# Performance work log

Measured on AMD Instinct MI355X. Metric: run time of the kernel, lower is better.

Reference implementation:

```python
import jax, jax.numpy as jnp
import numpy as np
from jax import lax

B, T, H, L = 8192, 1, 1024, 4  # batch, decode steps, hidden_size, n_layers


def _lstm_layer(c, h, xs, Wx, Wh, b):
    """Uni-directional LSTM over time axis. xs: [B, T, F]; c,h: [B, H].
    Returns final carry (c, h) and per-step hidden states [B, T, H]."""
    def step(carry, x_t):
        c, h = carry
        z = x_t @ Wx + h @ Wh + b              # [B, 4H]
        i, f, g, o = jnp.split(z, 4, axis=-1)
        i = jax.nn.sigmoid(i)
        f = jax.nn.sigmoid(f)
        g = jnp.tanh(g)
        o = jax.nn.sigmoid(o)
        c = f * c + i * g
        h = o * jnp.tanh(c)
        return (c, h), h
    (c, h), hs = lax.scan(step, (c, h), jnp.swapaxes(xs, 0, 1))  # scan over T
    return c, h, jnp.swapaxes(hs, 0, 1)        # [B, T, H]


def setup_inputs() -> dict:
    key = jax.random.key(0)
    ks = jax.random.split(key, 12)
    s = 0.02
    return {
        "x_todec": jax.random.normal(ks[0], (B, T), jnp.float32),
        "c0": jax.random.normal(ks[1], (B, H), jnp.float32),
        "h0": jax.random.normal(ks[2], (B, H), jnp.float32),
        # layer 0: input feature dim = 1 (x_todec expanded on axis 2)
        "Wx0": jax.random.normal(ks[3], (1, 4 * H), jnp.float32) * s,
        "Wh0": jax.random.normal(ks[4], (H, 4 * H), jnp.float32) * s,
        "b0": jnp.zeros((4 * H,), jnp.float32),
        # layers 1..L-1: input feature dim = H
        "Wx": jax.random.normal(ks[5], (L - 1, H, 4 * H), jnp.float32) * s,
        "Wh": jax.random.normal(ks[6], (L - 1, H, 4 * H), jnp.float32) * s,
        "b": jnp.zeros((L - 1, 4 * H), jnp.float32),
        # final prediction head Dense(features=1)
        "Wd": jax.random.normal(ks[7], (H, 1), jnp.float32) * s,
        "bd": jnp.zeros((1,), jnp.float32),
        "training": 0,
    }


def reference(x_todec, c0, h0, Wx0, Wh0, b0, Wx, Wh, b, Wd, bd, training):
    # training=0 -> nn.Dropout deterministic -> identity; omitted.
    x = x_todec[..., None]                      # [B, T, 1]
    c, h, xs = _lstm_layer(c0, h0, x, Wx0, Wh0, b0)
    for l in range(L - 1):                      # carry chains through layers
        c, h, xs = _lstm_layer(c, h, xs, Wx[l], Wh[l], b[l])
    x_pred = jnp.squeeze(xs @ Wd + bd, axis=-1)  # [B, T]
    return (c, h, x_pred)
```

## Files before the change

### kernel.cpp

```cpp
#include <hip/hip_runtime.h>
#include <hip/hip_bf16.h>


#define MB_  8192
#define HB_  1024
#define KB_  1024

typedef __attribute__((ext_vector_type(8))) short bf16x8;
typedef __attribute__((ext_vector_type(4))) float f32x4;

#define BAR()  asm volatile("s_barrier" ::: "memory")
#define VMW(n) asm volatile("s_waitcnt vmcnt(" #n ")" ::: "memory")

__device__ __forceinline__ void load_lds16(const void* g, void* l) {
  __builtin_amdgcn_global_load_lds(
      (const __attribute__((address_space(1))) unsigned int*)g,
      (__attribute__((address_space(3))) unsigned int*)l, 16, 0, 0);
}

__device__ __forceinline__ float sigmoidf_(float x) { return 1.0f / (1.0f + __expf(-x)); }
__device__ __forceinline__ float tanhf_fast(float x) { return 2.0f / (1.0f + __expf(-2.0f * x)) - 1.0f; }

__device__ __forceinline__ short f2bf(float f) {
  __hip_bfloat16 h = __float2bfloat16(f);
  return *(short*)&h;
}

__global__ __launch_bounds__(256) void cvt_f32_bf16(
    const float* __restrict__ in, __hip_bfloat16* __restrict__ out)
{
  const int i = blockIdx.x * 256 + threadIdx.x;
  const float4 f0 = ((const float4*)in)[i * 2];
  const float4 f1 = ((const float4*)in)[i * 2 + 1];
  bf16x8 v;
  v[0] = f2bf(f0.x); v[1] = f2bf(f0.y); v[2] = f2bf(f0.z); v[3] = f2bf(f0.w);
  v[4] = f2bf(f1.x); v[5] = f2bf(f1.y); v[6] = f2bf(f1.z); v[7] = f2bf(f1.w);
  ((bf16x8*)out)[i] = v;
}

__global__ __launch_bounds__(256) void prep_weights(
    const float* __restrict__ Wh0,
    const float* __restrict__ Wx,
    const float* __restrict__ Wh,
    __hip_bfloat16* __restrict__ WT)
{
  __shared__ float t[32][33];
  const int L  = blockIdx.z;
  const int n0 = blockIdx.x * 32;
  const int k0 = blockIdx.y * 32;
  const int tx = threadIdx.x & 31;
  const int ty = threadIdx.x >> 5;
  if (L == 0) {
    for (int kk = ty; kk < 32; kk += 8)
      t[kk][tx] = Wh0[(size_t)(k0 + kk) * 4096 + n0 + tx];
  } else {
    const float* wx = Wx + (size_t)(L - 1) * 1024 * 4096;
    const float* wh = Wh + (size_t)(L - 1) * 1024 * 4096;
    for (int kk = ty; kk < 32; kk += 8) {
      size_t idx = (size_t)(k0 + kk) * 4096 + n0 + tx;
      t[kk][tx] = wx[idx] + wh[idx];
    }
  }
  __syncthreads();
  __hip_bfloat16* dst = WT + (size_t)L * 4096 * 1024;
  for (int nn = ty; nn < 32; nn += 8)
    dst[(size_t)(n0 + nn) * 1024 + k0 + tx] = __float2bfloat16(t[tx][nn]);
}

template<bool FIRST, bool LAST>
__global__ __launch_bounds__(512, 2) void lstm_layer_kernel(
    const __hip_bfloat16* __restrict__ A,
    const __hip_bfloat16* __restrict__ WT,
    const float*          __restrict__ bias,
    const float*                       cin,
    float*                             cout,
    const float*          __restrict__ xvec,
    const float*          __restrict__ Wx0,
    void*                 __restrict__ hout)
{
  __shared__ __align__(16) char lds[131072];

  const int tid  = threadIdx.x;
  const int lane = tid & 63;
  const int wv   = tid >> 6;
  const int wr   = wv & 1;
  const int wc   = wv >> 1;
  const int l15  = lane & 15;
  const int lq   = lane >> 4;
  const int sw   = (l15 & 7) << 4;

  const int bid = blockIdx.x;
  const int sz  = (bid & 7) * 64 + (bid >> 3);
  const int m0  = (sz >> 4) * 256;
  const int n0h = (sz & 15) * 64;

  unsigned aoff[2][2], boff[2][2];
#pragma unroll
  for (int h = 0; h < 2; ++h)
#pragma unroll
    for (int j = 0; j < 2; ++j) {
      const int c    = j * 512 + tid;
      const int row  = c >> 3;
      const int colb = ((c & 7) ^ (row & 7)) << 4;
      aoff[h][j] = (unsigned)((m0 + h * 128 + row) * 2048 + colb);
      const int grow = (h * 2 + (row >> 6)) * 1024 + n0h + (row & 63);
      boff[h][j] = (unsigned)(grow * 2048 + colb);
    }
  const int ldsu = wv * 1024;
  const char* Ab = (const char*)A;
  const char* Wb = (const char*)WT;

  f32x4 acc[8][4] = {};

  auto stageA = [&](int h, int kt, int b) {
#pragma unroll
    for (int j = 0; j < 2; ++j)
      load_lds16(Ab + aoff[h][j] + kt * 128,
                 lds + b * 65536 + h * 16384 + j * 8192 + ldsu);
  };
  auto stageB = [&](int h, int kt, int b) {
#pragma unroll
    for (int j = 0; j < 2; ++j)
      load_lds16(Wb + boff[h][j] + kt * 128,
                 lds + b * 65536 + 32768 + h * 16384 + j * 8192 + ldsu);
  };
  auto quad = [&](int b, int sh, int gh) {
    const char* bA = lds + b * 65536 + wr * 16384;
    const char* bB = lds + b * 65536 + 32768 + gh * 16384;
    bf16x8 af[4][2], bfr[2][2];
#pragma unroll
    for (int i = 0; i < 4; ++i) {
      const int rl = (sh * 4 + i) * 16 + l15;
#pragma unroll
      for (int ks = 0; ks < 2; ++ks)
        af[i][ks] = *(const bf16x8*)(bA + rl * 128 + ((ks * 64 + lq * 16) ^ sw));
    }
#pragma unroll
    for (int g = 0; g < 2; ++g) {
      const int rb = g * 64 + wc * 16 + l15;
#pragma unroll
      for (int ks = 0; ks < 2; ++ks)
        bfr[g][ks] = *(const bf16x8*)(bB + rb * 128 + ((ks * 64 + lq * 16) ^ sw));
    }
    __builtin_amdgcn_s_setprio(1);
#pragma unroll
    for (int i = 0; i < 4; ++i)
#pragma unroll
      for (int g = 0; g < 2; ++g)
#pragma unroll
        for (int ks = 0; ks < 2; ++ks)
          acc[sh * 4 + i][gh * 2 + g] = __builtin_amdgcn_mfma_f32_16x16x32_bf16(
              af[i][ks], bfr[g][ks], acc[sh * 4 + i][gh * 2 + g], 0, 0, 0);
    __builtin_amdgcn_s_setprio(0);
  };

  stageA(0, 0, 0); stageA(1, 0, 0); stageB(0, 0, 0); stageB(1, 0, 0);

  for (int t = 0; t < 15; ++t) {
    const int cur = t & 1, nxt = cur ^ 1;
    VMW(2); BAR();
    stageA(0, t + 1, nxt); stageA(1, t + 1, nxt);
    quad(cur, 0, 0);
    BAR();
    stageB(0, t + 1, nxt);
    quad(cur, 1, 0);
    VMW(6); BAR();
    stageB(1, t + 1, nxt);
    quad(cur, 0, 1);
    BAR();
    quad(cur, 1, 1);
  }
  VMW(2); BAR();
  quad(1, 0, 0);
  quad(1, 1, 0);
  VMW(0); BAR();
  quad(1, 0, 1);
  quad(1, 1, 1);

  BAR();
  float* sC = (float*)lds;
  float* sH = (float*)(lds + 65536);

#pragma unroll
  for (int j = 0; j < 8; ++j) {
    const int idx = j * 512 + tid;
    const int row = idx >> 4;
    const int c4  = (idx & 15) << 2;
    load_lds16(cin + (size_t)(m0 + row) * HB_ + n0h + c4,
               (char*)sC + j * 8192 + ldsu);
  }

  const int jj  = n0h + wc * 16 + l15;
  const float bi  = bias[0 * HB_ + jj];
  const float bf_ = bias[1 * HB_ + jj];
  const float bg  = bias[2 * HB_ + jj];
  const float bo  = bias[3 * HB_ + jj];
  float wxi = 0.f, wxf = 0.f, wxg = 0.f, wxo = 0.f;
  if (FIRST) {
    wxi = Wx0[0 * HB_ + jj];
    wxf = Wx0[1 * HB_ + jj];
    wxg = Wx0[2 * HB_ + jj];
    wxo = Wx0[3 * HB_ + jj];
  }
  VMW(0); BAR();

  const int hl = wc * 16 + l15;
#pragma unroll
  for (int s = 0; s < 8; ++s) {
#pragma unroll
    for (int r = 0; r < 4; ++r) {
      const int mloc = wr * 128 + s * 16 + (lq << 2) + r;
      float zi = acc[s][0][r] + bi;
      float zf = acc[s][1][r] + bf_;
      float zg = acc[s][2][r] + bg;
      float zo = acc[s][3][r] + bo;
      if (FIRST) {
        const float xv = xvec[m0 + mloc];
        zi += xv * wxi; zf += xv * wxf; zg += xv * wxg; zo += xv * wxo;
      }
      const float ig = sigmoidf_(zi);
      const float fg = sigmoidf_(zf);
      const float gg = tanhf_fast(zg);
      const float og = sigmoidf_(zo);
      const float cn = fg * sC[mloc * 64 + hl] + ig * gg;
      const float hn = og * tanhf_fast(cn);
      sC[mloc * 64 + hl] = cn;
      sH[mloc * 64 + hl] = hn;
    }
  }
  BAR();

#pragma unroll
  for (int p = 0; p < 8; ++p) {
    const int idx = p * 512 + tid;
    const int row = idx >> 4, seg = idx & 15;
    *(float4*)(cout + (size_t)(m0 + row) * HB_ + n0h + seg * 4) =
        *(const float4*)&sC[row * 64 + seg * 4];
  }
  if (LAST) {
#pragma unroll
    for (int p = 0; p < 8; ++p) {
      const int idx = p * 512 + tid;
      const int row = idx >> 4, seg = idx & 15;
      *(float4*)((float*)hout + (size_t)(m0 + row) * HB_ + n0h + seg * 4) =
          *(const float4*)&sH[row * 64 + seg * 4];
    }
  } else {
#pragma unroll
    for (int p = 0; p < 4; ++p) {
      const int idx = p * 512 + tid;
      const int row = idx >> 3, seg = idx & 7;
      const float4 f0 = *(const float4*)&sH[row * 64 + seg * 8];
      const float4 f1 = *(const float4*)&sH[row * 64 + seg * 8 + 4];
      bf16x8 v;
      v[0] = f2bf(f0.x); v[1] = f2bf(f0.y); v[2] = f2bf(f0.z); v[3] = f2bf(f0.w);
      v[4] = f2bf(f1.x); v[5] = f2bf(f1.y); v[6] = f2bf(f1.z); v[7] = f2bf(f1.w);
      *(bf16x8*)((__hip_bfloat16*)hout + (size_t)(m0 + row) * HB_ + n0h + seg * 8) = v;
    }
  }
}

__global__ __launch_bounds__(256) void head_kernel(
    const float* __restrict__ h,
    const float* __restrict__ Wd,
    const float* __restrict__ bd,
    float* __restrict__ xpred)
{
  const int row  = blockIdx.x * 4 + (threadIdx.x >> 6);
  const int lane = threadIdx.x & 63;
  const float* hr = h + (size_t)row * HB_;
  float s = 0.f;
#pragma unroll
  for (int t = 0; t < 16; ++t) {
    const int k = t * 64 + lane;
    s += hr[k] * Wd[k];
  }
#pragma unroll
  for (int off = 32; off; off >>= 1) s += __shfl_down(s, off, 64);
  if (lane == 0) xpred[row] = s + bd[0];
}

extern "C" void kernel_launch(void* const* d_in, const int* in_sizes, int n_in,
                              void* d_out, int out_size, void* d_ws, size_t ws_size,
                              hipStream_t stream) {
  (void)in_sizes; (void)n_in; (void)out_size; (void)ws_size;
  const float* x   = (const float*)d_in[0];
  const float* c0  = (const float*)d_in[1];
  const float* h0  = (const float*)d_in[2];
  const float* Wx0 = (const float*)d_in[3];
  const float* Wh0 = (const float*)d_in[4];
  const float* b0  = (const float*)d_in[5];
  const float* Wx  = (const float*)d_in[6];
  const float* Wh  = (const float*)d_in[7];
  const float* b   = (const float*)d_in[8];
  const float* Wd  = (const float*)d_in[9];
  const float* bd  = (const float*)d_in[10];

  float* out_c = (float*)d_out;
  float* out_h = out_c + (size_t)MB_ * HB_;
  float* out_x = out_h + (size_t)MB_ * HB_;

  char* ws = (char*)d_ws;
  __hip_bfloat16* WT = (__hip_bfloat16*)ws;
  __hip_bfloat16* hA = (__hip_bfloat16*)(ws + (size_t)33554432);
  __hip_bfloat16* hB = (__hip_bfloat16*)(ws + (size_t)50331648);

  const size_t WTL = (size_t)4096 * 1024;

  prep_weights<<<dim3(128, 32, 4), 256, 0, stream>>>(Wh0, Wx, Wh, WT);
  cvt_f32_bf16<<<4096, 256, 0, stream>>>(h0, hA);

  lstm_layer_kernel<true,  false><<<512, 512, 0, stream>>>(
      hA, WT, b0, c0, out_c, x, Wx0, hB);
  lstm_layer_kernel<false, false><<<512, 512, 0, stream>>>(
      hB, WT + 1 * WTL, b + 0 * 4096, out_c, out_c, nullptr, nullptr, hA);
  lstm_layer_kernel<false, false><<<512, 512, 0, stream>>>(
      hA, WT + 2 * WTL, b + 1 * 4096, out_c, out_c, nullptr, nullptr, hB);
  lstm_layer_kernel<false, true><<<512, 512, 0, stream>>>(
      hB, WT + 3 * WTL, b + 2 * 4096, out_c, out_c, nullptr, nullptr, out_h);

  head_kernel<<<2048, 256, 0, stream>>>(out_h, Wd, bd, out_x);
}
```

Before: 610.2 us.

## Reorder MFMA quadrants to reuse B fragments and remap block tile order

Splits the per-quadrant LDS-read-plus-MFMA step into separate A and B fragment reads held in registers. Quadrants now run in an order that reuses the B fragments (0,0 then 0,1 then 1,1 then 1,0), which cuts redundant LDS reads, and the barriers and vmcnt waits are moved to overlap global-to-LDS staging with MFMA work. The epilogue's cell-state prefetch is issued before the last tile's MFMAs, and the block-to-tile mapping now walks the M dimension first to change which blocks share L2 data. Costs are more live registers and tighter wait counts, so a wrong vmcnt could create a data race.

Result: faster. 578.7 us (-5.2%).

```diff
diff --git a/kernel.cpp b/kernel.cpp
--- a/kernel.cpp
+++ b/kernel.cpp
@@ -91,8 +91,8 @@
 
   const int bid = blockIdx.x;
   const int sz  = (bid & 7) * 64 + (bid >> 3);
-  const int m0  = (sz >> 4) * 256;
-  const int n0h = (sz & 15) * 64;
+  const int m0  = (sz & 31) * 256;
+  const int n0h = (sz >> 5) * 64;
 
   unsigned aoff[2][2], boff[2][2];
 #pragma unroll
@@ -111,6 +111,8 @@
   const char* Wb = (const char*)WT;
 
   f32x4 acc[8][4] = {};
+  bf16x8 Af[4][2];
+  bf16x8 Bf0[2][2], Bf1[2][2];
 
   auto stageA = [&](int h, int kt, int b) {
 #pragma unroll
@@ -124,70 +126,85 @@
       load_lds16(Wb + boff[h][j] + kt * 128,
                  lds + b * 65536 + 32768 + h * 16384 + j * 8192 + ldsu);
   };
-  auto quad = [&](int b, int sh, int gh) {
-    const char* bA = lds + b * 65536 + wr * 16384;
-    const char* bB = lds + b * 65536 + 32768 + gh * 16384;
-    bf16x8 af[4][2], bfr[2][2];
+  auto readA = [&](const char* cb, int shalf) {
+    const char* bA = cb + wr * 16384;
 #pragma unroll
     for (int i = 0; i < 4; ++i) {
-      const int rl = (sh * 4 + i) * 16 + l15;
+      const int rl = (shalf * 4 + i) * 16 + l15;
 #pragma unroll
       for (int ks = 0; ks < 2; ++ks)
-        af[i][ks] = *(const bf16x8*)(bA + rl * 128 + ((ks * 64 + lq * 16) ^ sw));
-    }
+        Af[i][ks] = *(const bf16x8*)(bA + rl * 128 + ((ks * 64 + lq * 16) ^ sw));
+    }
+  };
+  auto readB = [&](const char* cb, int ghalf, bf16x8 Bf[2][2]) {
+    const char* bB = cb + 32768 + ghalf * 16384;
 #pragma unroll
     for (int g = 0; g < 2; ++g) {
       const int rb = g * 64 + wc * 16 + l15;
 #pragma unroll
       for (int ks = 0; ks < 2; ++ks)
-        bfr[g][ks] = *(const bf16x8*)(bB + rb * 128 + ((ks * 64 + lq * 16) ^ sw));
-    }
-    __builtin_amdgcn_s_setprio(1);
-#pragma unroll
-    for (int i = 0; i < 4; ++i)
-#pragma unroll
-      for (int g = 0; g < 2; ++g)
-#pragma unroll
-        for (int ks = 0; ks < 2; ++ks)
-          acc[sh * 4 + i][gh * 2 + g] = __builtin_amdgcn_mfma_f32_16x16x32_bf16(
-              af[i][ks], bfr[g][ks], acc[sh * 4 + i][gh * 2 + g], 0, 0, 0);
-    __builtin_amdgcn_s_setprio(0);
+        Bf[g][ks] = *(const bf16x8*)(bB + rb * 128 + ((ks * 64 + lq * 16) ^ sw));
+    }
   };
+
+#define MFMA16(SH, GH, BF)                                                    \
+  do {                                                                        \
+    __builtin_amdgcn_s_setprio(1);                                            \
+    _Pragma("unroll")                                                         \
+    for (int i_ = 0; i_ < 4; ++i_)                                            \
+      _Pragma("unroll")                                                       \
+      for (int g_ = 0; g_ < 2; ++g_)                                          \
+        _Pragma("unroll")                                                     \
+        for (int ks_ = 0; ks_ < 2; ++ks_)                                     \
+          acc[(SH) * 4 + i_][(GH) * 2 + g_] =                                 \
+              __builtin_amdgcn_mfma_f32_16x16x32_bf16(                        \
+                  Af[i_][ks_], BF[g_][ks_], acc[(SH) * 4 + i_][(GH) * 2 + g_],\
+                  0, 0, 0);                                                   \
+    __builtin_amdgcn_s_setprio(0);                                            \
+  } while (0)
 
   stageA(0, 0, 0); stageA(1, 0, 0); stageB(0, 0, 0); stageB(1, 0, 0);
 
   for (int t = 0; t < 15; ++t) {
     const int cur = t & 1, nxt = cur ^ 1;
+    const char* cb = lds + cur * 65536;
     VMW(2); BAR();
     stageA(0, t + 1, nxt); stageA(1, t + 1, nxt);
-    quad(cur, 0, 0);
-    BAR();
+    readA(cb, 0);
+    readB(cb, 0, Bf0);
+    BAR(); MFMA16(0, 0, Bf0);
+    VMW(4); BAR();
     stageB(0, t + 1, nxt);
-    quad(cur, 1, 0);
-    VMW(6); BAR();
+    readB(cb, 1, Bf1);
+    BAR(); MFMA16(0, 1, Bf1);
     stageB(1, t + 1, nxt);
-    quad(cur, 0, 1);
-    BAR();
-    quad(cur, 1, 1);
-  }
-  VMW(2); BAR();
-  quad(1, 0, 0);
-  quad(1, 1, 0);
-  VMW(0); BAR();
-  quad(1, 0, 1);
-  quad(1, 1, 1);
-
-  BAR();
+    readA(cb, 1);
+    BAR(); MFMA16(1, 1, Bf1);
+    BAR(); MFMA16(1, 0, Bf0);
+  }
+
   float* sC = (float*)lds;
   float* sH = (float*)(lds + 65536);
-
-#pragma unroll
-  for (int j = 0; j < 8; ++j) {
-    const int idx = j * 512 + tid;
-    const int row = idx >> 4;
-    const int c4  = (idx & 15) << 2;
-    load_lds16(cin + (size_t)(m0 + row) * HB_ + n0h + c4,
-               (char*)sC + j * 8192 + ldsu);
+  {
+    const char* cb = lds + 65536;
+    VMW(2); BAR();
+#pragma unroll
+    for (int j = 0; j < 8; ++j) {
+      const int idx = j * 512 + tid;
+      const int row = idx >> 4;
+      const int c4  = (idx & 15) << 2;
+      load_lds16(cin + (size_t)(m0 + row) * HB_ + n0h + c4,
+                 (char*)sC + j * 8192 + ldsu);
+    }
+    readA(cb, 0);
+    readB(cb, 0, Bf0);
+    BAR(); MFMA16(0, 0, Bf0);
+    VMW(8); BAR();
+    readB(cb, 1, Bf1);
+    BAR(); MFMA16(0, 1, Bf1);
+    readA(cb, 1);
+    BAR(); MFMA16(1, 1, Bf1);
+    BAR(); MFMA16(1, 0, Bf0);
   }
 
   const int jj  = n0h + wc * 16 + l15;
@@ -258,6 +275,7 @@
       *(bf16x8*)((__hip_bfloat16*)hout + (size_t)(m0 + row) * HB_ + n0h + seg * 8) = v;
     }
   }
+#undef MFMA16
 }
 
 __global__ __launch_bounds__(256) void head_kernel(
```

## Shrink LSTM GEMM tiles to 64x128 with 256-thread blocks and more workgroups

Applied to the files above, without the earlier changes.

Replaces the 256x256-output (4 gates x 64 hidden) tile per 512-thread block with a 64-row x 4x32-column tile per 256-thread block, launching 4096 workgroups instead of 512. The k-loop becomes a simple double-buffered stage/compute scheme using 48KB of LDS, and the cell state is read directly into registers rather than staged through LDS. The aim is higher occupancy and better load balance across CUs, at the cost of much lower operand reuse per tile, more global and L2 traffic for weights and activations, and an extra barrier per k-tile.

Result: no change. 601.3 us (-1.5%).

```diff
diff --git a/kernel.cpp b/kernel.cpp
--- a/kernel.cpp
+++ b/kernel.cpp
@@ -9,8 +9,9 @@
 typedef __attribute__((ext_vector_type(8))) short bf16x8;
 typedef __attribute__((ext_vector_type(4))) float f32x4;
 
-#define BAR()  asm volatile("s_barrier" ::: "memory")
-#define VMW(n) asm volatile("s_waitcnt vmcnt(" #n ")" ::: "memory")
+#define BAR()   asm volatile("s_barrier" ::: "memory")
+#define VMW(n)  asm volatile("s_waitcnt vmcnt(" #n ")" ::: "memory")
+#define LGKM0() asm volatile("s_waitcnt lgkmcnt(0)" ::: "memory")
 
 __device__ __forceinline__ void load_lds16(const void* g, void* l) {
   __builtin_amdgcn_global_load_lds(
@@ -68,7 +69,7 @@
 }
 
 template<bool FIRST, bool LAST>
-__global__ __launch_bounds__(512, 2) void lstm_layer_kernel(
+__global__ __launch_bounds__(256) void lstm_layer_kernel(
     const __hip_bfloat16* __restrict__ A,
     const __hip_bfloat16* __restrict__ WT,
     const float*          __restrict__ bias,
@@ -78,7 +79,7 @@
     const float*          __restrict__ Wx0,
     void*                 __restrict__ hout)
 {
-  __shared__ __align__(16) char lds[131072];
+  __shared__ __align__(16) char lds[49152];
 
   const int tid  = threadIdx.x;
   const int lane = tid & 63;
@@ -90,107 +91,92 @@
   const int sw   = (l15 & 7) << 4;
 
   const int bid = blockIdx.x;
-  const int sz  = (bid & 7) * 64 + (bid >> 3);
-  const int m0  = (sz >> 4) * 256;
-  const int n0h = (sz & 15) * 64;
-
-  unsigned aoff[2][2], boff[2][2];
-#pragma unroll
-  for (int h = 0; h < 2; ++h)
-#pragma unroll
-    for (int j = 0; j < 2; ++j) {
-      const int c    = j * 512 + tid;
-      const int row  = c >> 3;
-      const int colb = ((c & 7) ^ (row & 7)) << 4;
-      aoff[h][j] = (unsigned)((m0 + h * 128 + row) * 2048 + colb);
-      const int grow = (h * 2 + (row >> 6)) * 1024 + n0h + (row & 63);
-      boff[h][j] = (unsigned)(grow * 2048 + colb);
-    }
+  const int sz  = (bid & 7) * 512 + (bid >> 3);
+  const int n0h = (sz >> 7) * 32;
+  const int m0  = (sz & 127) * 64;
+
+  const int jj = n0h + wc * 16 + l15;
+
+  float cinv[2][4];
+#pragma unroll
+  for (int i = 0; i < 2; ++i)
+#pragma unroll
+    for (int r = 0; r < 4; ++r)
+      cinv[i][r] =
+          cin[(size_t)(m0 + wr * 32 + i * 16 + (lq << 2) + r) * HB_ + jj];
+
+  unsigned aoff[2], boff[4];
+#pragma unroll
+  for (int j = 0; j < 2; ++j) {
+    const int c    = j * 256 + tid;
+    const int row  = c >> 3;
+    const int colb = ((c & 7) ^ (row & 7)) << 4;
+    aoff[j] = (unsigned)((m0 + row) * 2048 + colb);
+  }
+#pragma unroll
+  for (int j = 0; j < 4; ++j) {
+    const int c    = j * 256 + tid;
+    const int row  = c >> 3;
+    const int colb = ((c & 7) ^ (row & 7)) << 4;
+    const int z    = (row >> 5) * 1024 + n0h + (row & 31);
+    boff[j] = (unsigned)(z * 2048 + colb);
+  }
   const int ldsu = wv * 1024;
   const char* Ab = (const char*)A;
   const char* Wb = (const char*)WT;
 
-  f32x4 acc[8][4] = {};
-
-  auto stageA = [&](int h, int kt, int b) {
+  f32x4 acc[2][4] = {};
+
+  auto stage = [&](int kt, char* buf) {
 #pragma unroll
     for (int j = 0; j < 2; ++j)
-      load_lds16(Ab + aoff[h][j] + kt * 128,
-                 lds + b * 65536 + h * 16384 + j * 8192 + ldsu);
+      load_lds16(Ab + aoff[j] + kt * 128, buf + j * 4096 + ldsu);
+#pragma unroll
+    for (int j = 0; j < 4; ++j)
+      load_lds16(Wb + boff[j] + kt * 128, buf + 8192 + j * 4096 + ldsu);
   };
-  auto stageB = [&](int h, int kt, int b) {
-#pragma unroll
-    for (int j = 0; j < 2; ++j)
-      load_lds16(Wb + boff[h][j] + kt * 128,
-                 lds + b * 65536 + 32768 + h * 16384 + j * 8192 + ldsu);
-  };
-  auto quad = [&](int b, int sh, int gh) {
-    const char* bA = lds + b * 65536 + wr * 16384;
-    const char* bB = lds + b * 65536 + 32768 + gh * 16384;
-    bf16x8 af[4][2], bfr[2][2];
-#pragma unroll
-    for (int i = 0; i < 4; ++i) {
-      const int rl = (sh * 4 + i) * 16 + l15;
+
+  auto ktile = [&](const char* buf) {
+    bf16x8 Af[2][2], Bf[4][2];
+#pragma unroll
+    for (int i = 0; i < 2; ++i) {
+      const int rl = wr * 32 + i * 16 + l15;
 #pragma unroll
       for (int ks = 0; ks < 2; ++ks)
-        af[i][ks] = *(const bf16x8*)(bA + rl * 128 + ((ks * 64 + lq * 16) ^ sw));
-    }
-#pragma unroll
-    for (int g = 0; g < 2; ++g) {
-      const int rb = g * 64 + wc * 16 + l15;
+        Af[i][ks] = *(const bf16x8*)(buf + rl * 128 + ((ks * 64 + lq * 16) ^ sw));
+    }
+#pragma unroll
+    for (int g = 0; g < 4; ++g) {
+      const int rb = g * 32 + wc * 16 + l15;
 #pragma unroll
       for (int ks = 0; ks < 2; ++ks)
-        bfr[g][ks] = *(const bf16x8*)(bB + rb * 128 + ((ks * 64 + lq * 16) ^ sw));
-    }
+        Bf[g][ks] = *(const bf16x8*)(buf + 8192 + rb * 128 +
+                                     ((ks * 64 + lq * 16) ^ sw));
+    }
+    LGKM0();
+    BAR();
     __builtin_amdgcn_s_setprio(1);
 #pragma unroll
-    for (int i = 0; i < 4; ++i)
-#pragma unroll
-      for (int g = 0; g < 2; ++g)
-#pragma unroll
-        for (int ks = 0; ks < 2; ++ks)
-          acc[sh * 4 + i][gh * 2 + g] = __builtin_amdgcn_mfma_f32_16x16x32_bf16(
-              af[i][ks], bfr[g][ks], acc[sh * 4 + i][gh * 2 + g], 0, 0, 0);
+    for (int ks = 0; ks < 2; ++ks)
+#pragma unroll
+      for (int i = 0; i < 2; ++i)
+#pragma unroll
+        for (int g = 0; g < 4; ++g)
+          acc[i][g] = __builtin_amdgcn_mfma_f32_16x16x32_bf16(
+              Af[i][ks], Bf[g][ks], acc[i][g], 0, 0, 0);
     __builtin_amdgcn_s_setprio(0);
   };
 
-  stageA(0, 0, 0); stageA(1, 0, 0); stageB(0, 0, 0); stageB(1, 0, 0);
+  stage(0, lds);
 
   for (int t = 0; t < 15; ++t) {
-    const int cur = t & 1, nxt = cur ^ 1;
-    VMW(2); BAR();
-    stageA(0, t + 1, nxt); stageA(1, t + 1, nxt);
-    quad(cur, 0, 0);
-    BAR();
-    stageB(0, t + 1, nxt);
-    quad(cur, 1, 0);
+    stage(t + 1, lds + ((t + 1) & 1) * 24576);
     VMW(6); BAR();
-    stageB(1, t + 1, nxt);
-    quad(cur, 0, 1);
-    BAR();
-    quad(cur, 1, 1);
-  }
-  VMW(2); BAR();
-  quad(1, 0, 0);
-  quad(1, 1, 0);
+    ktile(lds + (t & 1) * 24576);
+  }
   VMW(0); BAR();
-  quad(1, 0, 1);
-  quad(1, 1, 1);
-
-  BAR();
-  float* sC = (float*)lds;
-  float* sH = (float*)(lds + 65536);
-
-#pragma unroll
-  for (int j = 0; j < 8; ++j) {
-    const int idx = j * 512 + tid;
-    const int row = idx >> 4;
-    const int c4  = (idx & 15) << 2;
-    load_lds16(cin + (size_t)(m0 + row) * HB_ + n0h + c4,
-               (char*)sC + j * 8192 + ldsu);
-  }
-
-  const int jj  = n0h + wc * 16 + l15;
+  ktile(lds + 24576);
+
   const float bi  = bias[0 * HB_ + jj];
   const float bf_ = bias[1 * HB_ + jj];
   const float bg  = bias[2 * HB_ + jj];
@@ -202,18 +188,19 @@
     wxg = Wx0[2 * HB_ + jj];
     wxo = Wx0[3 * HB_ + jj];
   }
-  VMW(0); BAR();
-
+
+  float* sC = (float*)lds;
+  float* sH = (float*)(lds + 8192);
   const int hl = wc * 16 + l15;
 #pragma unroll
-  for (int s = 0; s < 8; ++s) {
+  for (int i = 0; i < 2; ++i) {
 #pragma unroll
     for (int r = 0; r < 4; ++r) {
-      const int mloc = wr * 128 + s * 16 + (lq << 2) + r;
-      float zi = acc[s][0][r] + bi;
-      float zf = acc[s][1][r] + bf_;
-      float zg = acc[s][2][r] + bg;
-      float zo = acc[s][3][r] + bo;
+      const int mloc = wr * 32 + i * 16 + (lq << 2) + r;
+      float zi = acc[i][0][r] + bi;
+      float zf = acc[i][1][r] + bf_;
+      float zg = acc[i][2][r] + bg;
+      float zo = acc[i][3][r] + bo;
       if (FIRST) {
         const float xv = xvec[m0 + mloc];
         zi += xv * wxi; zf += xv * wxf; zg += xv * wxg; zo += xv * wxo;
@@ -222,41 +209,37 @@
       const float fg = sigmoidf_(zf);
       const float gg = tanhf_fast(zg);
       const float og = sigmoidf_(zo);
-      const float cn = fg * sC[mloc * 64 + hl] + ig * gg;
+      const float cn = fg * cinv[i][r] + ig * gg;
       const float hn = og * tanhf_fast(cn);
-      sC[mloc * 64 + hl] = cn;
-      sH[mloc * 64 + hl] = hn;
-    }
-  }
-  BAR();
-
-#pragma unroll
-  for (int p = 0; p < 8; ++p) {
-    const int idx = p * 512 + tid;
-    const int row = idx >> 4, seg = idx & 15;
+      sC[mloc * 32 + hl] = cn;
+      sH[mloc * 32 + hl] = hn;
+    }
+  }
+  LGKM0(); BAR();
+
+#pragma unroll
+  for (int p = 0; p < 2; ++p) {
+    const int idx = p * 256 + tid;
+    const int row = idx >> 3, seg = idx & 7;
     *(float4*)(cout + (size_t)(m0 + row) * HB_ + n0h + seg * 4) =
-        *(const float4*)&sC[row * 64 + seg * 4];
+        *(const float4*)&sC[row * 32 + seg * 4];
   }
   if (LAST) {
 #pragma unroll
-    for (int p = 0; p < 8; ++p) {
-      const int idx = p * 512 + tid;
-      const int row = idx >> 4, seg = idx & 15;
+    for (int p = 0; p < 2; ++p) {
+      const int idx = p * 256 + tid;
+      const int row = idx >> 3, seg = idx & 7;
       *(float4*)((float*)hout + (size_t)(m0 + row) * HB_ + n0h + seg * 4) =
-          *(const float4*)&sH[row * 64 + seg * 4];
+          *(const float4*)&sH[row * 32 + seg * 4];
     }
   } else {
-#pragma unroll
-    for (int p = 0; p < 4; ++p) {
-      const int idx = p * 512 + tid;
-      const int row = idx >> 3, seg = idx & 7;
-      const float4 f0 = *(const float4*)&sH[row * 64 + seg * 8];
-      const float4 f1 = *(const float4*)&sH[row * 64 + seg * 8 + 4];
-      bf16x8 v;
-      v[0] = f2bf(f0.x); v[1] = f2bf(f0.y); v[2] = f2bf(f0.z); v[3] = f2bf(f0.w);
-      v[4] = f2bf(f1.x); v[5] = f2bf(f1.y); v[6] = f2bf(f1.z); v[7] = f2bf(f1.w);
-      *(bf16x8*)((__hip_bfloat16*)hout + (size_t)(m0 + row) * HB_ + n0h + seg * 8) = v;
-    }
+    const int row = tid >> 2, seg = tid & 3;
+    const float4 f0 = *(const float4*)&sH[row * 32 + seg * 8];
+    const float4 f1 = *(const float4*)&sH[row * 32 + seg * 8 + 4];
+    bf16x8 v;
+    v[0] = f2bf(f0.x); v[1] = f2bf(f0.y); v[2] = f2bf(f0.z); v[3] = f2bf(f0.w);
+    v[4] = f2bf(f1.x); v[5] = f2bf(f1.y); v[6] = f2bf(f1.z); v[7] = f2bf(f1.w);
+    *(bf16x8*)((__hip_bfloat16*)hout + (size_t)(m0 + row) * HB_ + n0h + seg * 8) = v;
   }
 }
 
@@ -310,13 +293,13 @@
   prep_weights<<<dim3(128, 32, 4), 256, 0, stream>>>(Wh0, Wx, Wh, WT);
   cvt_f32_bf16<<<4096, 256, 0, stream>>>(h0, hA);
 
-  lstm_layer_kernel<true,  false><<<512, 512, 0, stream>>>(
+  lstm_layer_kernel<true,  false><<<4096, 256, 0, stream>>>(
       hA, WT, b0, c0, out_c, x, Wx0, hB);
-  lstm_layer_kernel<false, false><<<512, 512, 0, stream>>>(
+  lstm_layer_kernel<false, false><<<4096, 256, 0, stream>>>(
       hB, WT + 1 * WTL, b + 0 * 4096, out_c, out_c, nullptr, nullptr, hA);
-  lstm_layer_kernel<false, false><<<512, 512, 0, stream>>>(
+  lstm_layer_kernel<false, false><<<4096, 256, 0, stream>>>(
       hA, WT + 2 * WTL, b + 1 * 4096, out_c, out_c, nullptr, nullptr, hB);
-  lstm_layer_kernel<false, true><<<512, 512, 0, stream>>>(
+  lstm_layer_kernel<false, true><<<4096, 256, 0, stream>>>(
       hB, WT + 3 * WTL, b + 2 * 4096, out_c, out_c, nullptr, nullptr, out_h);
 
   head_kernel<<<2048, 256, 0, stream>>>(out_h, Wd, bd, out_x);
```
